# Kernel optimization log

Hardware: AMD Instinct MI355X
Metric: run time of the kernel (lower is better)

## Reference

```python
import jax, jax.numpy as jnp
import numpy as np
from jax import lax

B, N, H, W = 1024, 5, 64, 64
D, NK, META_DIM = 24, 6, 16

def _lin(x, w, b):
    return x @ w.T + b

def _ln(x, g, b):
    m = x.mean(-1, keepdims=True)
    v = ((x - m) ** 2).mean(-1, keepdims=True)
    return (x - m) / jnp.sqrt(v + 1e-5) * g + b

def _conv(x, w, b):
    y = lax.conv_general_dilated(x, w, (1, 1), 'SAME', dimension_numbers=('NCHW', 'OIHW', 'NCHW'))
    return y + b[None, :, None, None]

def _maxpool2(x):
    return lax.reduce_window(x, -jnp.inf, lax.max, (1, 1, 2, 2), (1, 1, 2, 2), 'VALID')

def _fwd(centered_raw, meta, conv1_w, conv1_b, conv2_w, conv2_b, conv3_w, conv3_b, enc_fc_w, enc_fc_b,
         m1_w, m1_b, m2_w, m2_b, p1_w, p1_b, p2_w, p2_b, centers, arch_w, arch_b,
         in_proj_w, in_proj_b, out_proj_w, out_proj_b, ln1_g, ln1_b, ff1_w, ff1_b, ff2_w, ff2_b,
         ln2_g, ln2_b, rel1_w, rel1_b, rel2_w, rel2_b, s1_w, s1_b, s2_w, s2_b):
    Bn = centered_raw.shape[0]
    # --- TinyCNN encoder over B*N grayscale panels ---
    x = centered_raw.reshape(Bn * N, 1, H, W)
    h = _maxpool2(jax.nn.relu(_conv(x, conv1_w, conv1_b)))
    h = _maxpool2(jax.nn.relu(_conv(h, conv2_w, conv2_b)))
    h = jax.nn.relu(_conv(h, conv3_w, conv3_b))
    z_cen = _lin(h.mean((2, 3)), enc_fc_w, enc_fc_b).reshape(Bn, N, -1)  # [B,N,20]
    # --- meta MLP ---
    z_meta = _lin(jax.nn.relu(_lin(meta, m1_w, m1_b)), m2_w, m2_b)  # [B,N,12]
    # --- item projection ---
    h0 = _lin(jax.nn.relu(_lin(jnp.concatenate([z_cen, z_meta], -1), p1_w, p1_b)), p2_w, p2_b)  # [B,N,24]
    # --- archetype routing ---
    q = jax.nn.softmax(_lin(h0, arch_w, arch_b), axis=-1)  # [B,N,K]
    center = q @ centers
    coord = h0 - center
    # --- set attention block (dropout=0, eval mode) ---
    x0 = h0 + center
    qkv = _lin(x0, in_proj_w, in_proj_b)
    qh, kh, vh = jnp.split(qkv, 3, axis=-1)
    hd = D // 2  # 2 heads, head_dim=12
    qh = qh.reshape(Bn, N, 2, hd)
    kh = kh.reshape(Bn, N, 2, hd)
    vh = vh.reshape(Bn, N, 2, hd)
    scores = jnp.einsum('bqhd,bkhd->bhqk', qh, kh) / jnp.sqrt(jnp.float32(hd))
    attn = jax.nn.softmax(scores, axis=-1)
    a = jnp.einsum('bhqk,bkhd->bqhd', attn, vh).reshape(Bn, N, D)
    a = _lin(a, out_proj_w, out_proj_b)
    x1 = _ln(x0 + a, ln1_g, ln1_b)
    ff = _lin(jax.nn.relu(_lin(x1, ff1_w, ff1_b)), ff2_w, ff2_b)
    hset = _ln(x1 + ff, ln2_g, ln2_b)  # [B,N,24]
    # mean of other items (vectorized equivalent of the slice/concat loop)
    mean_other = (hset.sum(1, keepdims=True) - hset) / (N - 1)
    # --- pairwise relation aggregation ---
    xi = jnp.broadcast_to(hset[:, :, None, :], (Bn, N, N, D))
    xj = jnp.broadcast_to(hset[:, None, :, :], (Bn, N, N, D))
    cdiff = coord[:, :, None, :] - coord[:, None, :, :]
    q_overlap = (q[:, :, None, :] * q[:, None, :, :]).sum(-1, keepdims=True)
    d2 = (cdiff ** 2).sum(-1, keepdims=True)
    coord_dist = jnp.where(d2 > 0, jnp.sqrt(jnp.where(d2 > 0, d2, 1.0)), 0.0)  # safe norm
    feat = jnp.concatenate([xi, xj, jnp.abs(cdiff), q_overlap, coord_dist], -1)  # [B,N,N,74]
    rel = jax.nn.relu(_lin(jax.nn.relu(_lin(feat, rel1_w, rel1_b)), rel2_w, rel2_b))
    eye = jnp.eye(N, dtype=bool)[None, :, :, None]
    rel_mean = jnp.where(eye, 0.0, rel).sum(2) / (N - 1)
    rel_max = jnp.where(eye, -1e9, rel).max(2)
    # --- scorer (dropout=0, eval mode) ---
    sfeat = jnp.concatenate([h0, hset, center, coord, jnp.abs(hset - mean_other), rel_mean, rel_max, q], -1)  # [B,N,146]
    logits = _lin(jax.nn.relu(_lin(sfeat, s1_w, s1_b)), s2_w, s2_b)[..., 0]
    return logits, q

def setup_inputs() -> dict:
    key = jax.random.key(0)
    it = iter(jax.random.split(key, 50))
    def rn(shape, s=0.05):
        return jax.random.normal(next(it), shape, jnp.float32) * s
    inp = {
        'centered_raw': jax.random.normal(next(it), (B, N, H, W), jnp.float32),
        'meta': jax.random.normal(next(it), (B, N, META_DIM), jnp.float32),
        'conv1_w': rn((8, 1, 3, 3)), 'conv1_b': rn((8,)),
        'conv2_w': rn((12, 8, 3, 3)), 'conv2_b': rn((12,)),
        'conv3_w': rn((16, 12, 3, 3)), 'conv3_b': rn((16,)),
        'enc_fc_w': rn((20, 16)), 'enc_fc_b': rn((20,)),
        'm1_w': rn((12, META_DIM)), 'm1_b': rn((12,)),
        'm2_w': rn((12, 12)), 'm2_b': rn((12,)),
        'p1_w': rn((D, 32)), 'p1_b': rn((D,)),
        'p2_w': rn((D, D)), 'p2_b': rn((D,)),
        'centers': rn((NK, D), 0.02),
        'arch_w': rn((NK, D)), 'arch_b': rn((NK,)),
        'in_proj_w': rn((3 * D, D)), 'in_proj_b': rn((3 * D,)),
        'out_proj_w': rn((D, D)), 'out_proj_b': rn((D,)),
        'ln1_g': jnp.ones((D,), jnp.float32), 'ln1_b': jnp.zeros((D,), jnp.float32),
        'ff1_w': rn((2 * D, D)), 'ff1_b': rn((2 * D,)),
        'ff2_w': rn((D, 2 * D)), 'ff2_b': rn((D,)),
        'ln2_g': jnp.ones((D,), jnp.float32), 'ln2_b': jnp.zeros((D,), jnp.float32),
        'rel1_w': rn((10, 3 * D + 2)), 'rel1_b': rn((10,)),
        'rel2_w': rn((10, 10)), 'rel2_b': rn((10,)),
        's1_w': rn((40, 5 * D + 2 * 10 + NK)), 's1_b': rn((40,)),
        's2_w': rn((1, 40)), 's2_b': rn((1,)),
    }
    return inp

def reference(centered_raw, meta, conv1_w, conv1_b, conv2_w, conv2_b, conv3_w, conv3_b, enc_fc_w, enc_fc_b,
              m1_w, m1_b, m2_w, m2_b, p1_w, p1_b, p2_w, p2_b, centers, arch_w, arch_b,
              in_proj_w, in_proj_b, out_proj_w, out_proj_b, ln1_g, ln1_b, ff1_w, ff1_b, ff2_w, ff2_b,
              ln2_g, ln2_b, rel1_w, rel1_b, rel2_w, rel2_b, s1_w, s1_b, s2_w, s2_b):
    return _fwd(centered_raw, meta, conv1_w, conv1_b, conv2_w, conv2_b, conv3_w, conv3_b, enc_fc_w, enc_fc_b,
                m1_w, m1_b, m2_w, m2_b, p1_w, p1_b, p2_w, p2_b, centers, arch_w, arch_b,
                in_proj_w, in_proj_b, out_proj_w, out_proj_b, ln1_g, ln1_b, ff1_w, ff1_b, ff2_w, ff2_b,
                ln2_g, ln2_b, rel1_w, rel1_b, rel2_w, rel2_b, s1_w, s1_b, s2_w, s2_b)
```

## Files before the change

### kernel.cpp

```cpp
#include <hip/hip_runtime.h>
#include <hip/hip_bf16.h>


typedef __attribute__((ext_vector_type(8))) short bf16x8;
typedef __attribute__((ext_vector_type(4))) float f32x4;

static __device__ __forceinline__ unsigned short f2bfu(float f) {
    return __bfloat16_as_ushort(__float2bfloat16(f));
}

union CnnLds {
    float inBuf[66 * 66];
    unsigned short h1h2[34 * 34 * 8 + 18 * 18 * 16];
};

__global__ __launch_bounds__(256, 4)
void cnn_panel_kernel(const float* __restrict__ xin,
                      const float* __restrict__ c1w, const float* __restrict__ c1b,
                      const float* __restrict__ c2w, const float* __restrict__ c2b,
                      const float* __restrict__ c3w, const float* __restrict__ c3b,
                      float* __restrict__ pooled)
{
    __shared__ CnnLds U;
    float* const inBuf = U.inBuf;
    unsigned short* const h1 = U.h1h2;
    unsigned short* const h2 = U.h1h2 + 9248;

    const int tid = threadIdx.x;
    const int img = blockIdx.x;
    const int lane = tid & 63, wave = tid >> 6;

    float4 pan[4];
    {
        const float4* xv = (const float4*)(xin + (size_t)img * 4096);
        #pragma unroll
        for (int p = 0; p < 4; ++p) pan[p] = xv[tid + (p << 8)];
    }

    if (tid < 260) {
        int y, x;
        if (tid < 66)       { y = 0;         x = tid; }
        else if (tid < 132) { y = 65;        x = tid - 66; }
        else if (tid < 196) { y = tid - 131; x = 0; }
        else                { y = tid - 195; x = 65; }
        inBuf[y * 66 + x] = 0.0f;
    }
    for (int i = tid; i < (18 * 18 * 16) / 8; i += 256)
        ((uint4*)h2)[i] = make_uint4(0, 0, 0, 0);
    __syncthreads();

    #pragma unroll
    for (int p = 0; p < 4; ++p) {
        int i = tid + (p << 8);
        int base = i << 2, y = base >> 6, x = base & 63;
        float* dst = &inBuf[(y + 1) * 66 + (x + 1)];
        dst[0] = pan[p].x; dst[1] = pan[p].y; dst[2] = pan[p].z; dst[3] = pan[p].w;
    }
    __syncthreads();

    float c1out[4][8];
    #pragma unroll
    for (int p = 0; p < 4; ++p) {
        int pos = tid + (p << 8);
        int py = pos >> 5, px = pos & 31;
        float patch[4][4];
        #pragma unroll
        for (int dy = 0; dy < 4; ++dy)
            #pragma unroll
            for (int dx = 0; dx < 4; ++dx)
                patch[dy][dx] = inBuf[(2 * py + dy) * 66 + (2 * px + dx)];
        #pragma unroll
        for (int cp = 0; cp < 4; ++cp) {
            float2 bb = make_float2(c1b[2 * cp], c1b[2 * cp + 1]);
            float2 m = make_float2(-1e30f, -1e30f);
            #pragma unroll
            for (int ay = 0; ay < 2; ++ay)
                #pragma unroll
                for (int ax = 0; ax < 2; ++ax) {
                    float2 acc = bb;
                    #pragma unroll
                    for (int ky = 0; ky < 3; ++ky)
                        #pragma unroll
                        for (int kx = 0; kx < 3; ++kx) {
                            float pv = patch[ay + ky][ax + kx];
                            float2 w = make_float2(c1w[(2 * cp) * 9 + ky * 3 + kx],
                                                   c1w[(2 * cp + 1) * 9 + ky * 3 + kx]);
                            acc += make_float2(pv, pv) * w;
                        }
                    m.x = fmaxf(m.x, acc.x);
                    m.y = fmaxf(m.y, acc.y);
                }
            c1out[p][2 * cp]     = fmaxf(m.x, 0.0f);
            c1out[p][2 * cp + 1] = fmaxf(m.y, 0.0f);
        }
    }
    __syncthreads();

    #pragma unroll
    for (int p = 0; p < 4; ++p) {
        int pos = tid + (p << 8);
        int py = pos >> 5, px = pos & 31;
        uint4 v;
        v.x = (unsigned)f2bfu(c1out[p][0]) | ((unsigned)f2bfu(c1out[p][1]) << 16);
        v.y = (unsigned)f2bfu(c1out[p][2]) | ((unsigned)f2bfu(c1out[p][3]) << 16);
        v.z = (unsigned)f2bfu(c1out[p][4]) | ((unsigned)f2bfu(c1out[p][5]) << 16);
        v.w = (unsigned)f2bfu(c1out[p][6]) | ((unsigned)f2bfu(c1out[p][7]) << 16);
        *(uint4*)&h1[((py + 1) * 34 + (px + 1)) * 8] = v;
    }
    if (tid < 132) {
        int r = tid, y, x;
        if (r < 34)       { y = 0;      x = r; }
        else if (r < 68)  { y = 33;     x = r - 34; }
        else if (r < 100) { y = r - 67; x = 0; }
        else              { y = r - 99; x = 33; }
        *(uint4*)&h1[(y * 34 + x) * 8] = make_uint4(0, 0, 0, 0);
    }

    const int q = lane >> 4, mA = lane & 15, oc = lane & 15;
    int ky2[3], kx2[3];
    bf16x8 b2f[3];
    #pragma unroll
    for (int s = 0; s < 3; ++s) {
        int t = 4 * s + q;
        int tt = (t > 8) ? 4 : t;
        ky2[s] = tt / 3; kx2[s] = tt % 3;
        union { unsigned short us[8]; bf16x8 v; } bb;
        #pragma unroll
        for (int j = 0; j < 8; ++j)
            bb.us[j] = (t <= 8 && oc < 12) ? f2bfu(c2w[(oc * 8 + j) * 9 + t])
                                           : (unsigned short)0;
        b2f[s] = bb.v;
    }
    const float bias2 = (oc < 12) ? c2b[oc] : 0.0f;
    __syncthreads();

    for (int h = 0; h < 2; ++h) {
        #pragma unroll
        for (int Yi = 0; Yi < 4; ++Yi) {
            int Y = wave * 4 + Yi;
            float m0 = -1e30f, m1 = -1e30f;
            #pragma unroll
            for (int half = 0; half < 2; ++half) {
                int y = 2 * Y + half;
                f32x4 acc = {bias2, bias2, bias2, bias2};
                #pragma unroll
                for (int s = 0; s < 3; ++s) {
                    int off = ((y + ky2[s]) * 34 + (h * 16 + mA + kx2[s])) * 8;
                    bf16x8 a = *(const bf16x8*)&h1[off];
                    acc = __builtin_amdgcn_mfma_f32_16x16x32_bf16(a, b2f[s], acc, 0, 0, 0);
                }
                m0 = fmaxf(m0, fmaxf(acc[0], acc[1]));
                m1 = fmaxf(m1, fmaxf(acc[2], acc[3]));
            }
            if (oc < 12) {
                int X0 = h * 8 + q * 2;
                h2[((Y + 1) * 18 + (X0 + 1)) * 16 + oc] = f2bfu(fmaxf(m0, 0.0f));
                h2[((Y + 1) * 18 + (X0 + 2)) * 16 + oc] = f2bfu(fmaxf(m1, 0.0f));
            }
        }
    }
    __syncthreads();

    {
        const int hhalf = q & 1, tq = q >> 1;
        int ky3[5], kx3[5];
        bf16x8 b3f[5];
        #pragma unroll
        for (int s = 0; s < 5; ++s) {
            int slot = 2 * s + tq;
            int tt = (slot > 8) ? 4 : slot;
            ky3[s] = tt / 3; kx3[s] = tt % 3;
            union { unsigned short us[8]; bf16x8 v; } bb;
            #pragma unroll
            for (int j = 0; j < 8; ++j) {
                int ci = hhalf * 8 + j;
                bb.us[j] = (slot <= 8 && ci < 12) ? f2bfu(c3w[(oc * 12 + ci) * 9 + slot])
                                                  : (unsigned short)0;
            }
            b3f[s] = bb.v;
        }
        const float bias3 = c3b[oc];
        float psum = 0.0f;
        #pragma unroll
        for (int Yi = 0; Yi < 4; ++Yi) {
            int y = wave * 4 + Yi;
            f32x4 acc = {bias3, bias3, bias3, bias3};
            #pragma unroll
            for (int s = 0; s < 5; ++s) {
                int off = ((y + ky3[s]) * 18 + (mA + kx3[s])) * 16 + hhalf * 8;
                bf16x8 a = *(const bf16x8*)&h2[off];
                acc = __builtin_amdgcn_mfma_f32_16x16x32_bf16(a, b3f[s], acc, 0, 0, 0);
            }
            psum += fmaxf(acc[0], 0.0f) + fmaxf(acc[1], 0.0f)
                  + fmaxf(acc[2], 0.0f) + fmaxf(acc[3], 0.0f);
        }
        psum += __shfl_down(psum, 32);
        psum += __shfl_down(psum, 16);
        float* red = (float*)h1;
        if (lane < 16) red[lane * 4 + wave] = psum;
        __syncthreads();
        if (tid < 16) {
            float s = red[tid * 4] + red[tid * 4 + 1] + red[tid * 4 + 2] + red[tid * 4 + 3];
            pooled[(size_t)img * 16 + tid] = s * (1.0f / 256.0f);
        }
    }
}

struct RowS {
    float ph[5][16], mt[5][16];
    float zc[5][20], zmh[5][12], zm[5][12];
    float p1h[5][24], h0[5][24];
    float archl[5][6], q[5][6];
    float center[5][24], coord[5][24], x0[5][24];
    float qkv[5][72];
    float attn[2][5][5];
    float amix[5][24], aout[5][24], x1[5][24];
    float ffh[5][48], ff2o[5][24], hset[5][24], mo[5][24];
    float pq[20], pdist[20];
    float relh[20][10], relo[20][10];
    float rmean[5][10], rmax[5][10];
    float sfeat[5][146];
    float s1h[5][40];
};

__global__ __launch_bounds__(256)
void head_kernel(const float* __restrict__ pooled,
                 const float* __restrict__ meta,
                 const float* __restrict__ enc_fc_w, const float* __restrict__ enc_fc_b,
                 const float* __restrict__ m1_w, const float* __restrict__ m1_b,
                 const float* __restrict__ m2_w, const float* __restrict__ m2_b,
                 const float* __restrict__ p1_w, const float* __restrict__ p1_b,
                 const float* __restrict__ p2_w, const float* __restrict__ p2_b,
                 const float* __restrict__ centers,
                 const float* __restrict__ arch_w, const float* __restrict__ arch_b,
                 const float* __restrict__ in_proj_w, const float* __restrict__ in_proj_b,
                 const float* __restrict__ out_proj_w, const float* __restrict__ out_proj_b,
                 const float* __restrict__ ln1_g, const float* __restrict__ ln1_b,
                 const float* __restrict__ ff1_w, const float* __restrict__ ff1_b,
                 const float* __restrict__ ff2_w, const float* __restrict__ ff2_b,
                 const float* __restrict__ ln2_g, const float* __restrict__ ln2_b,
                 const float* __restrict__ rel1_w, const float* __restrict__ rel1_b,
                 const float* __restrict__ rel2_w, const float* __restrict__ rel2_b,
                 const float* __restrict__ s1_w, const float* __restrict__ s1_b,
                 const float* __restrict__ s2_w, const float* __restrict__ s2_b,
                 float* __restrict__ out, int q_off, int Bb)
{
    __shared__ RowS S[4];

    const int tid  = threadIdx.x;
    const int wid  = tid >> 6;
    const int lane = tid & 63;
    const int row  = blockIdx.x * 4 + wid;
    if (row >= Bb) return;

    RowS& H = S[wid];

    for (int i = lane; i < 80; i += 64) ((float*)H.ph)[i] = pooled[(size_t)row * 80 + i];
    for (int i = lane; i < 80; i += 64) ((float*)H.mt)[i] = meta[(size_t)row * 80 + i];

    for (int idx = lane; idx < 100; idx += 64) {
        int n = idx / 20, o = idx % 20;
        float a = enc_fc_b[o];
        #pragma unroll
        for (int k = 0; k < 16; ++k) a += H.ph[n][k] * enc_fc_w[o * 16 + k];
        H.zc[n][o] = a;
    }
    for (int idx = lane; idx < 60; idx += 64) {
        int n = idx / 12, o = idx % 12;
        float a = m1_b[o];
        #pragma unroll
        for (int k = 0; k < 16; ++k) a += H.mt[n][k] * m1_w[o * 16 + k];
        H.zmh[n][o] = fmaxf(a, 0.0f);
    }
    for (int idx = lane; idx < 60; idx += 64) {
        int n = idx / 12, o = idx % 12;
        float a = m2_b[o];
        #pragma unroll
        for (int k = 0; k < 12; ++k) a += H.zmh[n][k] * m2_w[o * 12 + k];
        H.zm[n][o] = a;
    }
    for (int idx = lane; idx < 120; idx += 64) {
        int n = idx / 24, o = idx % 24;
        float a = p1_b[o];
        #pragma unroll
        for (int k = 0; k < 20; ++k) a += H.zc[n][k] * p1_w[o * 32 + k];
        #pragma unroll
        for (int k = 0; k < 12; ++k) a += H.zm[n][k] * p1_w[o * 32 + 20 + k];
        H.p1h[n][o] = fmaxf(a, 0.0f);
    }
    for (int idx = lane; idx < 120; idx += 64) {
        int n = idx / 24, o = idx % 24;
        float a = p2_b[o];
        #pragma unroll
        for (int k = 0; k < 24; ++k) a += H.p1h[n][k] * p2_w[o * 24 + k];
        H.h0[n][o] = a;
    }
    for (int idx = lane; idx < 30; idx += 64) {
        int n = idx / 6, o = idx % 6;
        float a = arch_b[o];
        #pragma unroll
        for (int k = 0; k < 24; ++k) a += H.h0[n][k] * arch_w[o * 24 + k];
        H.archl[n][o] = a;
    }
    if (lane < 5) {
        int n = lane;
        float m = H.archl[n][0];
        #pragma unroll
        for (int k = 1; k < 6; ++k) m = fmaxf(m, H.archl[n][k]);
        float e[6], s = 0.0f;
        #pragma unroll
        for (int k = 0; k < 6; ++k) { e[k] = __expf(H.archl[n][k] - m); s += e[k]; }
        float inv = 1.0f / s;
        #pragma unroll
        for (int k = 0; k < 6; ++k) H.q[n][k] = e[k] * inv;
    }
    for (int idx = lane; idx < 120; idx += 64) {
        int n = idx / 24, d = idx % 24;
        float a = 0.0f;
        #pragma unroll
        for (int k = 0; k < 6; ++k) a += H.q[n][k] * centers[k * 24 + d];
        H.center[n][d] = a;
        H.coord[n][d] = H.h0[n][d] - a;
        H.x0[n][d] = H.h0[n][d] + a;
    }
    for (int idx = lane; idx < 360; idx += 64) {
        int n = idx / 72, o = idx % 72;
        float a = in_proj_b[o];
        #pragma unroll
        for (int k = 0; k < 24; ++k) a += H.x0[n][k] * in_proj_w[o * 24 + k];
        H.qkv[n][o] = a;
    }
    if (lane < 10) {
        int h = lane / 5, i = lane % 5;
        const float scale = 0.28867513459481287f;
        float sc[5], m = -1e30f;
        for (int j = 0; j < 5; ++j) {
            float a = 0.0f;
            #pragma unroll
            for (int d = 0; d < 12; ++d) a += H.qkv[i][h * 12 + d] * H.qkv[j][24 + h * 12 + d];
            sc[j] = a * scale;
            m = fmaxf(m, sc[j]);
        }
        float s = 0.0f;
        #pragma unroll
        for (int j = 0; j < 5; ++j) { sc[j] = __expf(sc[j] - m); s += sc[j]; }
        float inv = 1.0f / s;
        #pragma unroll
        for (int j = 0; j < 5; ++j) H.attn[h][i][j] = sc[j] * inv;
    }
    for (int idx = lane; idx < 120; idx += 64) {
        int i = idx / 24, o = idx % 24;
        int h = o / 12, d = o % 12;
        float a = 0.0f;
        #pragma unroll
        for (int j = 0; j < 5; ++j) a += H.attn[h][i][j] * H.qkv[j][48 + h * 12 + d];
        H.amix[i][o] = a;
    }
    for (int idx = lane; idx < 120; idx += 64) {
        int n = idx / 24, o = idx % 24;
        float a = out_proj_b[o];
        #pragma unroll
        for (int k = 0; k < 24; ++k) a += H.amix[n][k] * out_proj_w[o * 24 + k];
        H.aout[n][o] = H.x0[n][o] + a;
    }
    if (lane < 5) {
        int n = lane;
        float m = 0.0f;
        #pragma unroll
        for (int k = 0; k < 24; ++k) m += H.aout[n][k];
        m *= (1.0f / 24.0f);
        float v = 0.0f;
        #pragma unroll
        for (int k = 0; k < 24; ++k) { float d = H.aout[n][k] - m; v += d * d; }
        v *= (1.0f / 24.0f);
        float inv = 1.0f / sqrtf(v + 1e-5f);
        #pragma unroll
        for (int k = 0; k < 24; ++k)
            H.x1[n][k] = (H.aout[n][k] - m) * inv * ln1_g[k] + ln1_b[k];
    }
    for (int idx = lane; idx < 240; idx += 64) {
        int n = idx / 48, o = idx % 48;
        float a = ff1_b[o];
        #pragma unroll
        for (int k = 0; k < 24; ++k) a += H.x1[n][k] * ff1_w[o * 24 + k];
        H.ffh[n][o] = fmaxf(a, 0.0f);
    }
    for (int idx = lane; idx < 120; idx += 64) {
        int n = idx / 24, o = idx % 24;
        float a = ff2_b[o];
        #pragma unroll
        for (int k = 0; k < 48; ++k) a += H.ffh[n][k] * ff2_w[o * 48 + k];
        H.ff2o[n][o] = H.x1[n][o] + a;
    }
    if (lane < 5) {
        int n = lane;
        float m = 0.0f;
        #pragma unroll
        for (int k = 0; k < 24; ++k) m += H.ff2o[n][k];
        m *= (1.0f / 24.0f);
        float v = 0.0f;
        #pragma unroll
        for (int k = 0; k < 24; ++k) { float d = H.ff2o[n][k] - m; v += d * d; }
        v *= (1.0f / 24.0f);
        float inv = 1.0f / sqrtf(v + 1e-5f);
        #pragma unroll
        for (int k = 0; k < 24; ++k)
            H.hset[n][k] = (H.ff2o[n][k] - m) * inv * ln2_g[k] + ln2_b[k];
    }
    for (int idx = lane; idx < 120; idx += 64) {
        int n = idx / 24, d = idx % 24;
        float s = H.hset[0][d] + H.hset[1][d] + H.hset[2][d] + H.hset[3][d] + H.hset[4][d];
        H.mo[n][d] = (s - H.hset[n][d]) * 0.25f;
    }
    if (lane < 20) {
        int i = lane / 4, jj = lane % 4;
        int j = jj + (jj >= i ? 1 : 0);
        float qo = 0.0f;
        #pragma unroll
        for (int k = 0; k < 6; ++k) qo += H.q[i][k] * H.q[j][k];
        H.pq[lane] = qo;
        float d2 = 0.0f;
        #pragma unroll
        for (int k = 0; k < 24; ++k) { float d = H.coord[i][k] - H.coord[j][k]; d2 += d * d; }
        H.pdist[lane] = (d2 > 0.0f) ? sqrtf(d2) : 0.0f;
    }
    for (int idx = lane; idx < 200; idx += 64) {
        int p = idx / 10, c = idx % 10;
        int i = p / 4, jj = p % 4;
        int j = jj + (jj >= i ? 1 : 0);
        float a = rel1_b[c];
        const float* wr = rel1_w + c * 74;
        #pragma unroll
        for (int k = 0; k < 24; ++k) a += H.hset[i][k] * wr[k];
        #pragma unroll
        for (int k = 0; k < 24; ++k) a += H.hset[j][k] * wr[24 + k];
        #pragma unroll
        for (int k = 0; k < 24; ++k) a += fabsf(H.coord[i][k] - H.coord[j][k]) * wr[48 + k];
        a += H.pq[p] * wr[72];
        a += H.pdist[p] * wr[73];
        H.relh[p][c] = fmaxf(a, 0.0f);
    }
    for (int idx = lane; idx < 200; idx += 64) {
        int p = idx / 10, c = idx % 10;
        float a = rel2_b[c];
        #pragma unroll
        for (int k = 0; k < 10; ++k) a += H.relh[p][k] * rel2_w[c * 10 + k];
        H.relo[p][c] = fmaxf(a, 0.0f);
    }
    for (int idx = lane; idx < 50; idx += 64) {
        int i = idx / 10, c = idx % 10;
        float s = 0.0f, m = -1e30f;
        #pragma unroll
        for (int jj = 0; jj < 4; ++jj) {
            float v = H.relo[i * 4 + jj][c];
            s += v; m = fmaxf(m, v);
        }
        H.rmean[i][c] = s * 0.25f;
        H.rmax[i][c] = m;
    }
    for (int idx = lane; idx < 730; idx += 64) {
        int n = idx / 146, k = idx % 146;
        float v;
        if (k < 24)       v = H.h0[n][k];
        else if (k < 48)  v = H.hset[n][k - 24];
        else if (k < 72)  v = H.center[n][k - 48];
        else if (k < 96)  v = H.coord[n][k - 72];
        else if (k < 120) v = fabsf(H.hset[n][k - 96] - H.mo[n][k - 96]);
        else if (k < 130) v = H.rmean[n][k - 120];
        else if (k < 140) v = H.rmax[n][k - 130];
        else              v = H.q[n][k - 140];
        H.sfeat[n][k] = v;
    }
    for (int idx = lane; idx < 200; idx += 64) {
        int n = idx / 40, o = idx % 40;
        float a = s1_b[o];
        #pragma unroll 8
        for (int k = 0; k < 146; ++k) a += H.sfeat[n][k] * s1_w[o * 146 + k];
        H.s1h[n][o] = fmaxf(a, 0.0f);
    }
    if (lane < 5) {
        int n = lane;
        float a = s2_b[0];
        #pragma unroll
        for (int k = 0; k < 40; ++k) a += H.s1h[n][k] * s2_w[k];
        out[(size_t)row * 5 + n] = a;
    }
    if (lane < 30) {
        out[q_off + (size_t)row * 30 + lane] = H.q[lane / 6][lane % 6];
    }
}

extern "C" void kernel_launch(void* const* d_in, const int* in_sizes, int n_in,
                              void* d_out, int out_size, void* d_ws, size_t ws_size,
                              hipStream_t stream) {
    const int BN = in_sizes[0] / (64 * 64);
    const int Bb = BN / 5;

    float* pooled = (float*)d_ws;

    cnn_panel_kernel<<<BN, 256, 0, stream>>>(
        (const float*)d_in[0],
        (const float*)d_in[2], (const float*)d_in[3],
        (const float*)d_in[4], (const float*)d_in[5],
        (const float*)d_in[6], (const float*)d_in[7],
        pooled);

    head_kernel<<<(Bb + 3) / 4, 256, 0, stream>>>(
        pooled, (const float*)d_in[1],
        (const float*)d_in[8], (const float*)d_in[9],
        (const float*)d_in[10], (const float*)d_in[11],
        (const float*)d_in[12], (const float*)d_in[13],
        (const float*)d_in[14], (const float*)d_in[15],
        (const float*)d_in[16], (const float*)d_in[17],
        (const float*)d_in[18],
        (const float*)d_in[19], (const float*)d_in[20],
        (const float*)d_in[21], (const float*)d_in[22],
        (const float*)d_in[23], (const float*)d_in[24],
        (const float*)d_in[25], (const float*)d_in[26],
        (const float*)d_in[27], (const float*)d_in[28],
        (const float*)d_in[29], (const float*)d_in[30],
        (const float*)d_in[31], (const float*)d_in[32],
        (const float*)d_in[33], (const float*)d_in[34],
        (const float*)d_in[35], (const float*)d_in[36],
        (const float*)d_in[37], (const float*)d_in[38],
        (const float*)d_in[39], (const float*)d_in[40],
        (float*)d_out, BN, Bb);
}
```

Measured before the change: 321.2 us.

## Fuse CNN encoder and head into one kernel per row with prepacked MFMA fragments

The separate CNN-per-panel and head kernels are merged into one kernel where each block handles one batch row, running all 5 panels in sequence and then the head in wave 0. This removes the pooled-feature round trip through global memory and one launch. The conv2/conv3 weight fragments are converted to bf16 once by a small prep kernel and read back instead of being rebuilt per block. The conv1 stage also writes to LDS sooner via packed registers and uses float2 loads. The trade-off is that the grid drops from B*N blocks to B blocks, each doing 5x the serial work, and three waves sit idle during the head, which may hurt latency hiding.

```diff
diff --git a/kernel.cpp b/kernel.cpp
--- a/kernel.cpp
+++ b/kernel.cpp
@@ -7,204 +7,49 @@
 
 static __device__ __forceinline__ unsigned short f2bfu(float f) {
     return __bfloat16_as_ushort(__float2bfloat16(f));
+}
+
+__global__ __launch_bounds__(64)
+void prep_frags(const float* __restrict__ c2w, const float* __restrict__ c2b,
+                const float* __restrict__ c3w, const float* __restrict__ c3b,
+                float* __restrict__ fragbuf)
+{
+    const int lane = threadIdx.x;
+    const int q = lane >> 4, oc = lane & 15;
+    uint4* fb2 = (uint4*)fragbuf;
+    uint4* fb3 = (uint4*)fragbuf + 192;
+
+    #pragma unroll
+    for (int s = 0; s < 3; ++s) {
+        int t = 4 * s + q;
+        union { unsigned short us[8]; uint4 v; } bb;
+        #pragma unroll
+        for (int j = 0; j < 8; ++j)
+            bb.us[j] = (t <= 8 && oc < 12) ? f2bfu(c2w[(oc * 8 + j) * 9 + t])
+                                           : (unsigned short)0;
+        fb2[s * 64 + lane] = bb.v;
+    }
+    const int hhalf = q & 1, tq = q >> 1;
+    #pragma unroll
+    for (int s = 0; s < 5; ++s) {
+        int slot = 2 * s + tq;
+        union { unsigned short us[8]; uint4 v; } bb;
+        #pragma unroll
+        for (int j = 0; j < 8; ++j) {
+            int ci = hhalf * 8 + j;
+            bb.us[j] = (slot <= 8 && ci < 12) ? f2bfu(c3w[(oc * 12 + ci) * 9 + slot])
+                                              : (unsigned short)0;
+        }
+        fb3[s * 64 + lane] = bb.v;
+    }
+    fragbuf[2048 + lane] = (oc < 12) ? c2b[oc] : 0.0f;
+    fragbuf[2112 + lane] = c3b[oc];
 }
 
 union CnnLds {
     float inBuf[66 * 66];
     unsigned short h1h2[34 * 34 * 8 + 18 * 18 * 16];
 };
-
-__global__ __launch_bounds__(256, 4)
-void cnn_panel_kernel(const float* __restrict__ xin,
-                      const float* __restrict__ c1w, const float* __restrict__ c1b,
-                      const float* __restrict__ c2w, const float* __restrict__ c2b,
-                      const float* __restrict__ c3w, const float* __restrict__ c3b,
-                      float* __restrict__ pooled)
-{
-    __shared__ CnnLds U;
-    float* const inBuf = U.inBuf;
-    unsigned short* const h1 = U.h1h2;
-    unsigned short* const h2 = U.h1h2 + 9248;
-
-    const int tid = threadIdx.x;
-    const int img = blockIdx.x;
-    const int lane = tid & 63, wave = tid >> 6;
-
-    float4 pan[4];
-    {
-        const float4* xv = (const float4*)(xin + (size_t)img * 4096);
-        #pragma unroll
-        for (int p = 0; p < 4; ++p) pan[p] = xv[tid + (p << 8)];
-    }
-
-    if (tid < 260) {
-        int y, x;
-        if (tid < 66)       { y = 0;         x = tid; }
-        else if (tid < 132) { y = 65;        x = tid - 66; }
-        else if (tid < 196) { y = tid - 131; x = 0; }
-        else                { y = tid - 195; x = 65; }
-        inBuf[y * 66 + x] = 0.0f;
-    }
-    for (int i = tid; i < (18 * 18 * 16) / 8; i += 256)
-        ((uint4*)h2)[i] = make_uint4(0, 0, 0, 0);
-    __syncthreads();
-
-    #pragma unroll
-    for (int p = 0; p < 4; ++p) {
-        int i = tid + (p << 8);
-        int base = i << 2, y = base >> 6, x = base & 63;
-        float* dst = &inBuf[(y + 1) * 66 + (x + 1)];
-        dst[0] = pan[p].x; dst[1] = pan[p].y; dst[2] = pan[p].z; dst[3] = pan[p].w;
-    }
-    __syncthreads();
-
-    float c1out[4][8];
-    #pragma unroll
-    for (int p = 0; p < 4; ++p) {
-        int pos = tid + (p << 8);
-        int py = pos >> 5, px = pos & 31;
-        float patch[4][4];
-        #pragma unroll
-        for (int dy = 0; dy < 4; ++dy)
-            #pragma unroll
-            for (int dx = 0; dx < 4; ++dx)
-                patch[dy][dx] = inBuf[(2 * py + dy) * 66 + (2 * px + dx)];
-        #pragma unroll
-        for (int cp = 0; cp < 4; ++cp) {
-            float2 bb = make_float2(c1b[2 * cp], c1b[2 * cp + 1]);
-            float2 m = make_float2(-1e30f, -1e30f);
-            #pragma unroll
-            for (int ay = 0; ay < 2; ++ay)
-                #pragma unroll
-                for (int ax = 0; ax < 2; ++ax) {
-                    float2 acc = bb;
-                    #pragma unroll
-                    for (int ky = 0; ky < 3; ++ky)
-                        #pragma unroll
-                        for (int kx = 0; kx < 3; ++kx) {
-                            float pv = patch[ay + ky][ax + kx];
-                            float2 w = make_float2(c1w[(2 * cp) * 9 + ky * 3 + kx],
-                                                   c1w[(2 * cp + 1) * 9 + ky * 3 + kx]);
-                            acc += make_float2(pv, pv) * w;
-                        }
-                    m.x = fmaxf(m.x, acc.x);
-                    m.y = fmaxf(m.y, acc.y);
-                }
-            c1out[p][2 * cp]     = fmaxf(m.x, 0.0f);
-            c1out[p][2 * cp + 1] = fmaxf(m.y, 0.0f);
-        }
-    }
-    __syncthreads();
-
-    #pragma unroll
-    for (int p = 0; p < 4; ++p) {
-        int pos = tid + (p << 8);
-        int py = pos >> 5, px = pos & 31;
-        uint4 v;
-        v.x = (unsigned)f2bfu(c1out[p][0]) | ((unsigned)f2bfu(c1out[p][1]) << 16);
-        v.y = (unsigned)f2bfu(c1out[p][2]) | ((unsigned)f2bfu(c1out[p][3]) << 16);
-        v.z = (unsigned)f2bfu(c1out[p][4]) | ((unsigned)f2bfu(c1out[p][5]) << 16);
-        v.w = (unsigned)f2bfu(c1out[p][6]) | ((unsigned)f2bfu(c1out[p][7]) << 16);
-        *(uint4*)&h1[((py + 1) * 34 + (px + 1)) * 8] = v;
-    }
-    if (tid < 132) {
-        int r = tid, y, x;
-        if (r < 34)       { y = 0;      x = r; }
-        else if (r < 68)  { y = 33;     x = r - 34; }
-        else if (r < 100) { y = r - 67; x = 0; }
-        else              { y = r - 99; x = 33; }
-        *(uint4*)&h1[(y * 34 + x) * 8] = make_uint4(0, 0, 0, 0);
-    }
-
-    const int q = lane >> 4, mA = lane & 15, oc = lane & 15;
-    int ky2[3], kx2[3];
-    bf16x8 b2f[3];
-    #pragma unroll
-    for (int s = 0; s < 3; ++s) {
-        int t = 4 * s + q;
-        int tt = (t > 8) ? 4 : t;
-        ky2[s] = tt / 3; kx2[s] = tt % 3;
-        union { unsigned short us[8]; bf16x8 v; } bb;
-        #pragma unroll
-        for (int j = 0; j < 8; ++j)
-            bb.us[j] = (t <= 8 && oc < 12) ? f2bfu(c2w[(oc * 8 + j) * 9 + t])
-                                           : (unsigned short)0;
-        b2f[s] = bb.v;
-    }
-    const float bias2 = (oc < 12) ? c2b[oc] : 0.0f;
-    __syncthreads();
-
-    for (int h = 0; h < 2; ++h) {
-        #pragma unroll
-        for (int Yi = 0; Yi < 4; ++Yi) {
-            int Y = wave * 4 + Yi;
-            float m0 = -1e30f, m1 = -1e30f;
-            #pragma unroll
-            for (int half = 0; half < 2; ++half) {
-                int y = 2 * Y + half;
-                f32x4 acc = {bias2, bias2, bias2, bias2};
-                #pragma unroll
-                for (int s = 0; s < 3; ++s) {
-                    int off = ((y + ky2[s]) * 34 + (h * 16 + mA + kx2[s])) * 8;
-                    bf16x8 a = *(const bf16x8*)&h1[off];
-                    acc = __builtin_amdgcn_mfma_f32_16x16x32_bf16(a, b2f[s], acc, 0, 0, 0);
-                }
-                m0 = fmaxf(m0, fmaxf(acc[0], acc[1]));
-                m1 = fmaxf(m1, fmaxf(acc[2], acc[3]));
-            }
-            if (oc < 12) {
-                int X0 = h * 8 + q * 2;
-                h2[((Y + 1) * 18 + (X0 + 1)) * 16 + oc] = f2bfu(fmaxf(m0, 0.0f));
-                h2[((Y + 1) * 18 + (X0 + 2)) * 16 + oc] = f2bfu(fmaxf(m1, 0.0f));
-            }
-        }
-    }
-    __syncthreads();
-
-    {
-        const int hhalf = q & 1, tq = q >> 1;
-        int ky3[5], kx3[5];
-        bf16x8 b3f[5];
-        #pragma unroll
-        for (int s = 0; s < 5; ++s) {
-            int slot = 2 * s + tq;
-            int tt = (slot > 8) ? 4 : slot;
-            ky3[s] = tt / 3; kx3[s] = tt % 3;
-            union { unsigned short us[8]; bf16x8 v; } bb;
-            #pragma unroll
-            for (int j = 0; j < 8; ++j) {
-                int ci = hhalf * 8 + j;
-                bb.us[j] = (slot <= 8 && ci < 12) ? f2bfu(c3w[(oc * 12 + ci) * 9 + slot])
-                                                  : (unsigned short)0;
-            }
-            b3f[s] = bb.v;
-        }
-        const float bias3 = c3b[oc];
-        float psum = 0.0f;
-        #pragma unroll
-        for (int Yi = 0; Yi < 4; ++Yi) {
-            int y = wave * 4 + Yi;
-            f32x4 acc = {bias3, bias3, bias3, bias3};
-            #pragma unroll
-            for (int s = 0; s < 5; ++s) {
-                int off = ((y + ky3[s]) * 18 + (mA + kx3[s])) * 16 + hhalf * 8;
-                bf16x8 a = *(const bf16x8*)&h2[off];
-                acc = __builtin_amdgcn_mfma_f32_16x16x32_bf16(a, b3f[s], acc, 0, 0, 0);
-            }
-            psum += fmaxf(acc[0], 0.0f) + fmaxf(acc[1], 0.0f)
-                  + fmaxf(acc[2], 0.0f) + fmaxf(acc[3], 0.0f);
-        }
-        psum += __shfl_down(psum, 32);
-        psum += __shfl_down(psum, 16);
-        float* red = (float*)h1;
-        if (lane < 16) red[lane * 4 + wave] = psum;
-        __syncthreads();
-        if (tid < 16) {
-            float s = red[tid * 4] + red[tid * 4 + 1] + red[tid * 4 + 2] + red[tid * 4 + 3];
-            pooled[(size_t)img * 16 + tid] = s * (1.0f / 256.0f);
-        }
-    }
-}
 
 struct RowS {
     float ph[5][16], mt[5][16];
@@ -223,39 +68,261 @@
     float s1h[5][40];
 };
 
-__global__ __launch_bounds__(256)
-void head_kernel(const float* __restrict__ pooled,
-                 const float* __restrict__ meta,
-                 const float* __restrict__ enc_fc_w, const float* __restrict__ enc_fc_b,
-                 const float* __restrict__ m1_w, const float* __restrict__ m1_b,
-                 const float* __restrict__ m2_w, const float* __restrict__ m2_b,
-                 const float* __restrict__ p1_w, const float* __restrict__ p1_b,
-                 const float* __restrict__ p2_w, const float* __restrict__ p2_b,
-                 const float* __restrict__ centers,
-                 const float* __restrict__ arch_w, const float* __restrict__ arch_b,
-                 const float* __restrict__ in_proj_w, const float* __restrict__ in_proj_b,
-                 const float* __restrict__ out_proj_w, const float* __restrict__ out_proj_b,
-                 const float* __restrict__ ln1_g, const float* __restrict__ ln1_b,
-                 const float* __restrict__ ff1_w, const float* __restrict__ ff1_b,
-                 const float* __restrict__ ff2_w, const float* __restrict__ ff2_b,
-                 const float* __restrict__ ln2_g, const float* __restrict__ ln2_b,
-                 const float* __restrict__ rel1_w, const float* __restrict__ rel1_b,
-                 const float* __restrict__ rel2_w, const float* __restrict__ rel2_b,
-                 const float* __restrict__ s1_w, const float* __restrict__ s1_b,
-                 const float* __restrict__ s2_w, const float* __restrict__ s2_b,
-                 float* __restrict__ out, int q_off, int Bb)
+union FusedLds { CnnLds U; RowS H; };
+
+template <bool PREP>
+__global__ __launch_bounds__(256, 4)
+void fused_kernel(const float* __restrict__ xin,
+                  const float* __restrict__ meta,
+                  const float* __restrict__ c1w, const float* __restrict__ c1b,
+                  const float* __restrict__ c2w, const float* __restrict__ c2b,
+                  const float* __restrict__ c3w, const float* __restrict__ c3b,
+                  const float* __restrict__ fragbuf,
+                  const float* __restrict__ enc_fc_w, const float* __restrict__ enc_fc_b,
+                  const float* __restrict__ m1_w, const float* __restrict__ m1_b,
+                  const float* __restrict__ m2_w, const float* __restrict__ m2_b,
+                  const float* __restrict__ p1_w, const float* __restrict__ p1_b,
+                  const float* __restrict__ p2_w, const float* __restrict__ p2_b,
+                  const float* __restrict__ centers,
+                  const float* __restrict__ arch_w, const float* __restrict__ arch_b,
+                  const float* __restrict__ in_proj_w, const float* __restrict__ in_proj_b,
+                  const float* __restrict__ out_proj_w, const float* __restrict__ out_proj_b,
+                  const float* __restrict__ ln1_g, const float* __restrict__ ln1_b,
+                  const float* __restrict__ ff1_w, const float* __restrict__ ff1_b,
+                  const float* __restrict__ ff2_w, const float* __restrict__ ff2_b,
+                  const float* __restrict__ ln2_g, const float* __restrict__ ln2_b,
+                  const float* __restrict__ rel1_w, const float* __restrict__ rel1_b,
+                  const float* __restrict__ rel2_w, const float* __restrict__ rel2_b,
+                  const float* __restrict__ s1_w, const float* __restrict__ s1_b,
+                  const float* __restrict__ s2_w, const float* __restrict__ s2_b,
+                  float* __restrict__ out, int q_off)
 {
-    __shared__ RowS S[4];
-
-    const int tid  = threadIdx.x;
-    const int wid  = tid >> 6;
-    const int lane = tid & 63;
-    const int row  = blockIdx.x * 4 + wid;
-    if (row >= Bb) return;
-
-    RowS& H = S[wid];
-
-    for (int i = lane; i < 80; i += 64) ((float*)H.ph)[i] = pooled[(size_t)row * 80 + i];
+    __shared__ FusedLds UH;
+    __shared__ float pooled5[5][16];
+
+    float* const inBuf = UH.U.inBuf;
+    unsigned short* const h1 = UH.U.h1h2;
+    unsigned short* const h2 = UH.U.h1h2 + 9248;
+
+    const int tid = threadIdx.x;
+    const int row = blockIdx.x;
+    const int lane = tid & 63, wave = tid >> 6;
+
+    for (int pimg = 0; pimg < 5; ++pimg) {
+        const int img = row * 5 + pimg;
+
+        float4 pan[4];
+        {
+            const float4* xv = (const float4*)(xin + (size_t)img * 4096);
+            #pragma unroll
+            for (int p = 0; p < 4; ++p) pan[p] = xv[tid + (p << 8)];
+        }
+
+        if (tid < 260) {
+            int y, x;
+            if (tid < 66)       { y = 0;         x = tid; }
+            else if (tid < 132) { y = 65;        x = tid - 66; }
+            else if (tid < 196) { y = tid - 131; x = 0; }
+            else                { y = tid - 195; x = 65; }
+            inBuf[y * 66 + x] = 0.0f;
+        }
+        for (int i = tid; i < (18 * 18 * 16) / 8; i += 256)
+            ((uint4*)h2)[i] = make_uint4(0, 0, 0, 0);
+        __syncthreads();
+
+        #pragma unroll
+        for (int p = 0; p < 4; ++p) {
+            int i = tid + (p << 8);
+            int base = i << 2, y = base >> 6, x = base & 63;
+            float* dst = &inBuf[(y + 1) * 66 + (x + 1)];
+            dst[0] = pan[p].x; dst[1] = pan[p].y; dst[2] = pan[p].z; dst[3] = pan[p].w;
+        }
+        __syncthreads();
+
+        uint4 h1pack[4];
+        #pragma unroll
+        for (int p = 0; p < 4; ++p) {
+            int pos = tid + (p << 8);
+            int py = pos >> 5, px = pos & 31;
+            float patch[4][4];
+            {
+                const float* pb = &inBuf[(2 * py) * 66 + (2 * px)];
+                #pragma unroll
+                for (int dy = 0; dy < 4; ++dy) {
+                    float2 a = *(const float2*)&pb[dy * 66];
+                    float2 b = *(const float2*)&pb[dy * 66 + 2];
+                    patch[dy][0] = a.x; patch[dy][1] = a.y;
+                    patch[dy][2] = b.x; patch[dy][3] = b.y;
+                }
+            }
+            float c1o[8];
+            #pragma unroll
+            for (int cp = 0; cp < 4; ++cp) {
+                float2 bb = make_float2(c1b[2 * cp], c1b[2 * cp + 1]);
+                float2 m = make_float2(-1e30f, -1e30f);
+                #pragma unroll
+                for (int ay = 0; ay < 2; ++ay)
+                    #pragma unroll
+                    for (int ax = 0; ax < 2; ++ax) {
+                        float2 acc = bb;
+                        #pragma unroll
+                        for (int ky = 0; ky < 3; ++ky)
+                            #pragma unroll
+                            for (int kx = 0; kx < 3; ++kx) {
+                                float pv = patch[ay + ky][ax + kx];
+                                float2 w = make_float2(c1w[(2 * cp) * 9 + ky * 3 + kx],
+                                                       c1w[(2 * cp + 1) * 9 + ky * 3 + kx]);
+                                acc += make_float2(pv, pv) * w;
+                            }
+                        m.x = fmaxf(m.x, acc.x);
+                        m.y = fmaxf(m.y, acc.y);
+                    }
+                c1o[2 * cp]     = fmaxf(m.x, 0.0f);
+                c1o[2 * cp + 1] = fmaxf(m.y, 0.0f);
+            }
+            uint4 v;
+            v.x = (unsigned)f2bfu(c1o[0]) | ((unsigned)f2bfu(c1o[1]) << 16);
+            v.y = (unsigned)f2bfu(c1o[2]) | ((unsigned)f2bfu(c1o[3]) << 16);
+            v.z = (unsigned)f2bfu(c1o[4]) | ((unsigned)f2bfu(c1o[5]) << 16);
+            v.w = (unsigned)f2bfu(c1o[6]) | ((unsigned)f2bfu(c1o[7]) << 16);
+            h1pack[p] = v;
+        }
+        __syncthreads();
+
+        #pragma unroll
+        for (int p = 0; p < 4; ++p) {
+            int pos = tid + (p << 8);
+            int py = pos >> 5, px = pos & 31;
+            *(uint4*)&h1[((py + 1) * 34 + (px + 1)) * 8] = h1pack[p];
+        }
+        if (tid < 132) {
+            int r = tid, y, x;
+            if (r < 34)       { y = 0;      x = r; }
+            else if (r < 68)  { y = 33;     x = r - 34; }
+            else if (r < 100) { y = r - 67; x = 0; }
+            else              { y = r - 99; x = 33; }
+            *(uint4*)&h1[(y * 34 + x) * 8] = make_uint4(0, 0, 0, 0);
+        }
+
+        const int q = lane >> 4, mA = lane & 15, oc = lane & 15;
+        int ky2[3], kx2[3];
+        #pragma unroll
+        for (int s = 0; s < 3; ++s) {
+            int t = 4 * s + q;
+            int tt = (t > 8) ? 4 : t;
+            ky2[s] = tt / 3; kx2[s] = tt % 3;
+        }
+        bf16x8 b2f[3];
+        float bias2;
+        if constexpr (PREP) {
+            const uint4* fb2 = (const uint4*)fragbuf;
+            #pragma unroll
+            for (int s = 0; s < 3; ++s) b2f[s] = *(const bf16x8*)&fb2[s * 64 + lane];
+            bias2 = fragbuf[2048 + lane];
+        } else {
+            #pragma unroll
+            for (int s = 0; s < 3; ++s) {
+                int t = 4 * s + q;
+                union { unsigned short us[8]; bf16x8 v; } bb;
+                #pragma unroll
+                for (int j = 0; j < 8; ++j)
+                    bb.us[j] = (t <= 8 && oc < 12) ? f2bfu(c2w[(oc * 8 + j) * 9 + t])
+                                                   : (unsigned short)0;
+                b2f[s] = bb.v;
+            }
+            bias2 = (oc < 12) ? c2b[oc] : 0.0f;
+        }
+        __syncthreads();
+
+        for (int h = 0; h < 2; ++h) {
+            #pragma unroll
+            for (int Yi = 0; Yi < 4; ++Yi) {
+                int Y = wave * 4 + Yi;
+                float m0 = -1e30f, m1 = -1e30f;
+                #pragma unroll
+                for (int half = 0; half < 2; ++half) {
+                    int y = 2 * Y + half;
+                    f32x4 acc = {bias2, bias2, bias2, bias2};
+                    #pragma unroll
+                    for (int s = 0; s < 3; ++s) {
+                        int off = ((y + ky2[s]) * 34 + (h * 16 + mA + kx2[s])) * 8;
+                        bf16x8 a = *(const bf16x8*)&h1[off];
+                        acc = __builtin_amdgcn_mfma_f32_16x16x32_bf16(a, b2f[s], acc, 0, 0, 0);
+                    }
+                    m0 = fmaxf(m0, fmaxf(acc[0], acc[1]));
+                    m1 = fmaxf(m1, fmaxf(acc[2], acc[3]));
+                }
+                if (oc < 12) {
+                    int X0 = h * 8 + q * 2;
+                    h2[((Y + 1) * 18 + (X0 + 1)) * 16 + oc] = f2bfu(fmaxf(m0, 0.0f));
+                    h2[((Y + 1) * 18 + (X0 + 2)) * 16 + oc] = f2bfu(fmaxf(m1, 0.0f));
+                }
+            }
+        }
+        __syncthreads();
+
+        {
+            const int hhalf = q & 1, tq = q >> 1;
+            int ky3[5], kx3[5];
+            #pragma unroll
+            for (int s = 0; s < 5; ++s) {
+                int slot = 2 * s + tq;
+                int tt = (slot > 8) ? 4 : slot;
+                ky3[s] = tt / 3; kx3[s] = tt % 3;
+            }
+            bf16x8 b3f[5];
+            float bias3;
+            if constexpr (PREP) {
+                const uint4* fb3 = (const uint4*)fragbuf + 192;
+                #pragma unroll
+                for (int s = 0; s < 5; ++s) b3f[s] = *(const bf16x8*)&fb3[s * 64 + lane];
+                bias3 = fragbuf[2112 + lane];
+            } else {
+                #pragma unroll
+                for (int s = 0; s < 5; ++s) {
+                    int slot = 2 * s + tq;
+                    union { unsigned short us[8]; bf16x8 v; } bb;
+                    #pragma unroll
+                    for (int j = 0; j < 8; ++j) {
+                        int ci = hhalf * 8 + j;
+                        bb.us[j] = (slot <= 8 && ci < 12) ? f2bfu(c3w[(oc * 12 + ci) * 9 + slot])
+                                                          : (unsigned short)0;
+                    }
+                    b3f[s] = bb.v;
+                }
+                bias3 = c3b[oc];
+            }
+            float psum = 0.0f;
+            #pragma unroll
+            for (int Yi = 0; Yi < 4; ++Yi) {
+                int y = wave * 4 + Yi;
+                f32x4 acc = {bias3, bias3, bias3, bias3};
+                #pragma unroll
+                for (int s = 0; s < 5; ++s) {
+                    int off = ((y + ky3[s]) * 18 + (mA + kx3[s])) * 16 + hhalf * 8;
+                    bf16x8 a = *(const bf16x8*)&h2[off];
+                    acc = __builtin_amdgcn_mfma_f32_16x16x32_bf16(a, b3f[s], acc, 0, 0, 0);
+                }
+                psum += fmaxf(acc[0], 0.0f) + fmaxf(acc[1], 0.0f)
+                      + fmaxf(acc[2], 0.0f) + fmaxf(acc[3], 0.0f);
+            }
+            psum += __shfl_down(psum, 32);
+            psum += __shfl_down(psum, 16);
+            float* red = (float*)h1;
+            if (lane < 16) red[lane * 4 + wave] = psum;
+            __syncthreads();
+            if (tid < 16) {
+                float s = red[tid * 4] + red[tid * 4 + 1] + red[tid * 4 + 2] + red[tid * 4 + 3];
+                pooled5[pimg][tid] = s * (1.0f / 256.0f);
+            }
+            __syncthreads();
+        }
+    }
+
+    if (wave != 0) return;
+    RowS& H = UH.H;
+
+    for (int i = lane; i < 80; i += 64) ((float*)H.ph)[i] = ((const float*)pooled5)[i];
     for (int i = lane; i < 80; i += 64) ((float*)H.mt)[i] = meta[(size_t)row * 80 + i];
 
     for (int idx = lane; idx < 100; idx += 64) {
@@ -496,33 +563,42 @@
     const int BN = in_sizes[0] / (64 * 64);
     const int Bb = BN / 5;
 
-    float* pooled = (float*)d_ws;
-
-    cnn_panel_kernel<<<BN, 256, 0, stream>>>(
-        (const float*)d_in[0],
-        (const float*)d_in[2], (const float*)d_in[3],
-        (const float*)d_in[4], (const float*)d_in[5],
-        (const float*)d_in[6], (const float*)d_in[7],
-        pooled);
-
-    head_kernel<<<(Bb + 3) / 4, 256, 0, stream>>>(
-        pooled, (const float*)d_in[1],
-        (const float*)d_in[8], (const float*)d_in[9],
-        (const float*)d_in[10], (const float*)d_in[11],
-        (const float*)d_in[12], (const float*)d_in[13],
-        (const float*)d_in[14], (const float*)d_in[15],
-        (const float*)d_in[16], (const float*)d_in[17],
-        (const float*)d_in[18],
-        (const float*)d_in[19], (const float*)d_in[20],
-        (const float*)d_in[21], (const float*)d_in[22],
-        (const float*)d_in[23], (const float*)d_in[24],
-        (const float*)d_in[25], (const float*)d_in[26],
-        (const float*)d_in[27], (const float*)d_in[28],
-        (const float*)d_in[29], (const float*)d_in[30],
-        (const float*)d_in[31], (const float*)d_in[32],
-        (const float*)d_in[33], (const float*)d_in[34],
-        (const float*)d_in[35], (const float*)d_in[36],
-        (const float*)d_in[37], (const float*)d_in[38],
-        (const float*)d_in[39], (const float*)d_in[40],
-        (float*)d_out, BN, Bb);
+    float* fragbuf = (float*)d_ws;
+    const bool use_prep = ws_size >= 8704;
+
+    if (use_prep)
+        prep_frags<<<1, 64, 0, stream>>>(
+            (const float*)d_in[4], (const float*)d_in[5],
+            (const float*)d_in[6], (const float*)d_in[7], fragbuf);
+
+    #define FUSED_ARGS \
+        (const float*)d_in[0], (const float*)d_in[1], \
+        (const float*)d_in[2], (const float*)d_in[3], \
+        (const float*)d_in[4], (const float*)d_in[5], \
+        (const float*)d_in[6], (const float*)d_in[7], \
+        fragbuf, \
+        (const float*)d_in[8], (const float*)d_in[9], \
+        (const float*)d_in[10], (const float*)d_in[11], \
+        (const float*)d_in[12], (const float*)d_in[13], \
+        (const float*)d_in[14], (const float*)d_in[15], \
+        (const float*)d_in[16], (const float*)d_in[17], \
+        (const float*)d_in[18], \
+        (const float*)d_in[19], (const float*)d_in[20], \
+        (const float*)d_in[21], (const float*)d_in[22], \
+        (const float*)d_in[23], (const float*)d_in[24], \
+        (const float*)d_in[25], (const float*)d_in[26], \
+        (const float*)d_in[27], (const float*)d_in[28], \
+        (const float*)d_in[29], (const float*)d_in[30], \
+        (const float*)d_in[31], (const float*)d_in[32], \
+        (const float*)d_in[33], (const float*)d_in[34], \
+        (const float*)d_in[35], (const float*)d_in[36], \
+        (const float*)d_in[37], (const float*)d_in[38], \
+        (const float*)d_in[39], (const float*)d_in[40], \
+        (float*)d_out, BN
+
+    if (use_prep)
+        fused_kernel<true><<<Bb, 256, 0, stream>>>(FUSED_ARGS);
+    else
+        fused_kernel<false><<<Bb, 256, 0, stream>>>(FUSED_ARGS);
+    #undef FUSED_ARGS
 }
```

New measurement: 379.5 us. 18.1% more time.
